# Optimization experiments

Measured on AMD Instinct MI355X. Metric: run time of the kernel, lower is better.

## Reference

```python
import jax, jax.numpy as jnp
import numpy as np

T_THRESH = 1.0  # t_thresh init arg


def _step_fn(x):
    # Heaviside forward (gradient handled separately in bwd module)
    return (x > 0).astype(x.dtype)


def setup_inputs() -> dict:
    key = jax.random.key(0)
    k1, = jax.random.split(key, 1)
    x = jax.random.normal(k1, (64, 500, 1024), dtype=jnp.float32)
    w_input = jnp.asarray(1.0, dtype=jnp.float32)
    w_leak = jnp.asarray(0.1, dtype=jnp.float32)
    return {"x": x, "w_input": w_input, "w_leak": w_leak}


def reference(x, w_input, w_leak):
    # Leaky integrate-and-fire over time axis (axis=1).
    # Vm_t = relu(w_i * x_t + (1 - w_l) * Vm_{t-1} * step(t_thresh - Vm_{t-1}))
    # spike_t = step(Vm_t - t_thresh)
    def step(Vm, xt):  # Vm, xt: [B, C]
        forget = _step_fn(T_THRESH - Vm)  # reset if Vm crossed threshold
        Vm = jax.nn.relu(w_input * xt + (1.0 - w_leak) * Vm * forget)
        spike = _step_fn(Vm - T_THRESH)
        return Vm, spike

    Vm0 = jnp.zeros_like(x[:, 0])  # [B, C]
    xt = jnp.swapaxes(x, 0, 1)  # [T, B, C]
    _, spikes = jax.lax.scan(step, Vm0, xt)
    return jnp.swapaxes(spikes, 0, 1)  # [B, T, C]
```

## Files before the change

### kernel.cpp

```cpp
#include <hip/hip_runtime.h>


#define LIF_B 64
#define LIF_T 500
#define LIF_C 1024
#define LIF_TC 20
#define LIF_NCH 25
#define LIF_NBUF 4

typedef float vfloat4 __attribute__((ext_vector_type(4)));

#define GLOBAL_AS(p) ((__attribute__((address_space(1))) const void*)(uintptr_t)(p))
#define LDS_AS(p)    ((__attribute__((address_space(3))) void*)(uintptr_t)(p))

#define VMWAIT(n) asm volatile("s_waitcnt vmcnt(" #n ")" ::: "memory")
#define LGKM0()   asm volatile("s_waitcnt lgkmcnt(0)" ::: "memory")
#define BARRIER() do { __builtin_amdgcn_s_barrier(); asm volatile("" ::: "memory"); } while (0)

__global__ __launch_bounds__(512) void lif_kernel(
    const float* __restrict__ x,
    const float* __restrict__ w_input_p,
    const float* __restrict__ w_leak_p,
    float* __restrict__ out) {

  __shared__ __align__(16) float lds_x[LIF_NBUF][4][LIF_TC * 64];
  __shared__ __align__(16) float sp[4][4 * 64];

  const int b     = blockIdx.x >> 2;
  const int cbase = (blockIdx.x & 3) << 8;
  const int tidx  = threadIdx.x;
  const int wave  = tidx >> 6;
  const int lane  = tidx & 63;
  const bool producer = wave < 4;
  const int w = wave & 3;

  const float wi = w_input_p[0];
  const float kl = __fsub_rn(1.0f, w_leak_p[0]);
  asm volatile("s_waitcnt vmcnt(0) lgkmcnt(0)" ::: "memory");

  const float* xblk = x   + (size_t)b * LIF_T * LIF_C + cbase;
  float*       oblk = out + (size_t)b * LIF_T * LIF_C + cbase;

  auto stage = [&](int k, int p) {
    const float* src0 = xblk + (size_t)k * LIF_TC * LIF_C
                      + (w << 6) + ((lane & 15) << 2);
#pragma unroll
    for (int r0 = 0; r0 < LIF_TC; r0 += 4) {
      const float* g = src0 + (size_t)(r0 + (lane >> 4)) * LIF_C;
      float* l = &lds_x[p][w][r0 * 64];
      __builtin_amdgcn_global_load_lds(GLOBAL_AS(g), LDS_AS(l), 16, 0, 0);
    }
    __builtin_amdgcn_sched_barrier(0);
  };

  float Vm = 0.0f;

  if (producer) { stage(0, 0); stage(1, 1); stage(2, 2); }

  for (int k = 0; k < LIF_NCH; ++k) {
    if (producer) {
      if (k <= LIF_NCH - 3)      VMWAIT(10);
      else if (k == LIF_NCH - 2) VMWAIT(5);
      else                       VMWAIT(0);
    } else {
      LGKM0();
    }
    BARRIER();

    if (producer) {
      if (k + 3 < LIF_NCH) stage(k + 3, (k + 3) & 3);
    } else {
      const int p = k & 3;
      float* obase = oblk + (size_t)k * LIF_TC * LIF_C + (w << 6);
#pragma unroll
      for (int r0 = 0; r0 < LIF_TC; r0 += 4) {
#pragma unroll
        for (int dr = 0; dr < 4; ++dr) {
          const float xt  = lds_x[p][w][(r0 + dr) * 64 + lane];
          const float acc = (Vm < 1.0f) ? __fmul_rn(kl, Vm) : 0.0f;
          const float v   = __fadd_rn(__fmul_rn(wi, xt), acc);
          Vm = fmaxf(v, 0.0f);
          sp[w][dr * 64 + lane] = (Vm > 1.0f) ? 1.0f : 0.0f;
        }
        const vfloat4 v4 =
            *reinterpret_cast<const vfloat4*>(&sp[w][lane << 2]);
        float* gdst = obase + (size_t)(r0 + (lane >> 4)) * LIF_C
                    + ((lane & 15) << 2);
        __builtin_nontemporal_store(v4, reinterpret_cast<vfloat4*>(gdst));
      }
      __builtin_amdgcn_sched_barrier(0);
    }
  }
}

extern "C" void kernel_launch(void* const* d_in, const int* in_sizes, int n_in,
                              void* d_out, int out_size, void* d_ws, size_t ws_size,
                              hipStream_t stream) {
  const float* x  = (const float*)d_in[0];
  const float* wi = (const float*)d_in[1];
  const float* wl = (const float*)d_in[2];
  float* out = (float*)d_out;

  const int grid = LIF_B * (LIF_C / 256);
  lif_kernel<<<grid, 512, 0, stream>>>(x, wi, wl, out);
}
```

Measured before the change: 233.7 us.

## Replace producer/consumer waves with per-wave self-staging deeper prefetch pipeline

Removes the split into producer and consumer waves and the block-wide barriers. Each of the four waves now stages its own slice of x into LDS through async global-to-LDS loads and consumes it itself, so the only ordering needed is vmcnt waits. The buffer ring grows from 4 to 7 chunks, keeping about six chunks of loads in flight, and the block shrinks to 256 threads. The risks are that LDS use rises to about 143 KB per block, which limits occupancy, and that the vmcnt thresholds must also account for the interleaved stores.

```diff
diff --git a/kernel.cpp b/kernel.cpp
--- a/kernel.cpp
+++ b/kernel.cpp
@@ -6,7 +6,7 @@
 #define LIF_C 1024
 #define LIF_TC 20
 #define LIF_NCH 25
-#define LIF_NBUF 4
+#define LIF_NBUF 7
 
 typedef float vfloat4 __attribute__((ext_vector_type(4)));
 
@@ -14,10 +14,8 @@
 #define LDS_AS(p)    ((__attribute__((address_space(3))) void*)(uintptr_t)(p))
 
 #define VMWAIT(n) asm volatile("s_waitcnt vmcnt(" #n ")" ::: "memory")
-#define LGKM0()   asm volatile("s_waitcnt lgkmcnt(0)" ::: "memory")
-#define BARRIER() do { __builtin_amdgcn_s_barrier(); asm volatile("" ::: "memory"); } while (0)
 
-__global__ __launch_bounds__(512) void lif_kernel(
+__global__ __launch_bounds__(256) void lif_kernel(
     const float* __restrict__ x,
     const float* __restrict__ w_input_p,
     const float* __restrict__ w_leak_p,
@@ -29,10 +27,8 @@
   const int b     = blockIdx.x >> 2;
   const int cbase = (blockIdx.x & 3) << 8;
   const int tidx  = threadIdx.x;
-  const int wave  = tidx >> 6;
+  const int w     = tidx >> 6;
   const int lane  = tidx & 63;
-  const bool producer = wave < 4;
-  const int w = wave & 3;
 
   const float wi = w_input_p[0];
   const float kl = __fsub_rn(1.0f, w_leak_p[0]);
@@ -55,42 +51,51 @@
 
   float Vm = 0.0f;
 
-  if (producer) { stage(0, 0); stage(1, 1); stage(2, 2); }
+  auto compute = [&](int k, int p) {
+    float* obase = oblk + (size_t)k * LIF_TC * LIF_C + (w << 6);
+#pragma unroll
+    for (int r0 = 0; r0 < LIF_TC; r0 += 4) {
+#pragma unroll
+      for (int dr = 0; dr < 4; ++dr) {
+        const float xt  = lds_x[p][w][(r0 + dr) * 64 + lane];
+        const float acc = (Vm < 1.0f) ? __fmul_rn(kl, Vm) : 0.0f;
+        const float v   = __fadd_rn(__fmul_rn(wi, xt), acc);
+        Vm = fmaxf(v, 0.0f);
+        sp[w][dr * 64 + lane] = (Vm > 1.0f) ? 1.0f : 0.0f;
+      }
+      const vfloat4 v4 =
+          *reinterpret_cast<const vfloat4*>(&sp[w][lane << 2]);
+      float* gdst = obase + (size_t)(r0 + (lane >> 4)) * LIF_C
+                  + ((lane & 15) << 2);
+      __builtin_nontemporal_store(v4, reinterpret_cast<vfloat4*>(gdst));
+    }
+    __builtin_amdgcn_sched_barrier(0);
+  };
 
-  for (int k = 0; k < LIF_NCH; ++k) {
-    if (producer) {
-      if (k <= LIF_NCH - 3)      VMWAIT(10);
-      else if (k == LIF_NCH - 2) VMWAIT(5);
-      else                       VMWAIT(0);
-    } else {
-      LGKM0();
-    }
-    BARRIER();
+  stage(0, 0); stage(1, 1); stage(2, 2);
+  stage(3, 3); stage(4, 4); stage(5, 5);
 
-    if (producer) {
-      if (k + 3 < LIF_NCH) stage(k + 3, (k + 3) & 3);
-    } else {
-      const int p = k & 3;
-      float* obase = oblk + (size_t)k * LIF_TC * LIF_C + (w << 6);
-#pragma unroll
-      for (int r0 = 0; r0 < LIF_TC; r0 += 4) {
-#pragma unroll
-        for (int dr = 0; dr < 4; ++dr) {
-          const float xt  = lds_x[p][w][(r0 + dr) * 64 + lane];
-          const float acc = (Vm < 1.0f) ? __fmul_rn(kl, Vm) : 0.0f;
-          const float v   = __fadd_rn(__fmul_rn(wi, xt), acc);
-          Vm = fmaxf(v, 0.0f);
-          sp[w][dr * 64 + lane] = (Vm > 1.0f) ? 1.0f : 0.0f;
-        }
-        const vfloat4 v4 =
-            *reinterpret_cast<const vfloat4*>(&sp[w][lane << 2]);
-        float* gdst = obase + (size_t)(r0 + (lane >> 4)) * LIF_C
-                    + ((lane & 15) << 2);
-        __builtin_nontemporal_store(v4, reinterpret_cast<vfloat4*>(gdst));
-      }
-      __builtin_amdgcn_sched_barrier(0);
+  VMWAIT(25);
+  stage(6, 6);
+  compute(0, 0);
+
+  {
+    int ps = 6, pc = 0;
+    for (int k = 1; k <= 18; ++k) {
+      VMWAIT(30);
+      if (++ps == LIF_NBUF) ps = 0;
+      stage(k + 6, ps);
+      if (++pc == LIF_NBUF) pc = 0;
+      compute(k, pc);
     }
   }
+
+  VMWAIT(30); compute(19, 5);
+  VMWAIT(25); compute(20, 6);
+  VMWAIT(20); compute(21, 0);
+  VMWAIT(15); compute(22, 1);
+  VMWAIT(10); compute(23, 2);
+  VMWAIT(5);  compute(24, 3);
 }
 
 extern "C" void kernel_launch(void* const* d_in, const int* in_sizes, int n_in,
@@ -102,5 +107,5 @@
   float* out = (float*)d_out;
 
   const int grid = LIF_B * (LIF_C / 256);
-  lif_kernel<<<grid, 512, 0, stream>>>(x, wi, wl, out);
+  lif_kernel<<<grid, 256, 0, stream>>>(x, wi, wl, out);
 }
```

Result: no change. 235.3 us (+0.7%).
